# Optimization experiments

Hardware: AMD Instinct MI355X
Metric: run time of the kernel (lower is better)

The kernel has to match this reference:

```python
import jax, jax.numpy as jnp
import numpy as np

B, H, W, D, C = 2, 128, 128, 8, 64
HEADS, DIM_HEAD = 4, 16
F_IN = C * D            # 512
F_OUT = DIM_HEAD * HEADS * D  # 512


def setup_inputs() -> dict:
    key = jax.random.key(0)
    ks = jax.random.split(key, 8)
    s = 0.02
    return {
        "x_in": jax.random.normal(ks[0], (B, H, W, D, C), dtype=jnp.float32),
        "Wq": jax.random.normal(ks[1], (F_IN, F_OUT), dtype=jnp.float32) * s,
        "Wk": jax.random.normal(ks[2], (F_IN, F_OUT), dtype=jnp.float32) * s,
        "Wv": jax.random.normal(ks[3], (F_IN, F_OUT), dtype=jnp.float32) * s,
        "rescale": jnp.ones((HEADS, 1, 1), dtype=jnp.float32),
        "Wp": jax.random.normal(ks[4], (F_OUT, F_IN), dtype=jnp.float32) * s,
        "bp": jnp.zeros((F_IN,), dtype=jnp.float32),
        "pos_w1": jax.random.normal(ks[5], (C, 1, 3, 3, 3), dtype=jnp.float32) * s,
        "pos_w2": jax.random.normal(ks[6], (C, 1, 3, 3, 3), dtype=jnp.float32) * s,
    }


def _dwconv3d(y, kern, groups):
    # y: [b,c,d,h,w], kern: [c,1,3,3,3] depthwise
    return jax.lax.conv_general_dilated(
        y, kern, window_strides=(1, 1, 1), padding="SAME",
        feature_group_count=groups,
        dimension_numbers=("NCDHW", "OIDHW", "NCDHW"))


def reference(x_in, Wq, Wk, Wv, rescale, Wp, bp, pos_w1, pos_w2):
    b, h, w, d, c = x_in.shape
    heads = rescale.shape[0]
    n = h * w
    x = x_in.reshape(b, n, d * c)
    q_inp = x @ Wq
    k_inp = x @ Wk
    v_inp = x @ Wv

    def split(t):  # [b,n,heads*Dh] -> [b,heads,Dh,n]  (Dh = dim_head*num_frm)
        return t.reshape(b, n, heads, -1).transpose(0, 2, 3, 1)

    q, k, v = split(q_inp), split(k_inp), split(v_inp)
    # L2-normalize along spatial axis n (last dim), torch F.normalize eps=1e-12
    q = q / jnp.maximum(jnp.linalg.norm(q, axis=-1, keepdims=True), 1e-12)
    k = k / jnp.maximum(jnp.linalg.norm(k, axis=-1, keepdims=True), 1e-12)
    # channel attention: [b,heads,Dh,Dh]
    attn = jnp.einsum("bhdn,bhen->bhde", k, q) * rescale
    attn = jax.nn.softmax(attn, axis=-1)
    out = jnp.einsum("bhde,bhen->bhdn", attn, v)  # [b,heads,Dh,n]
    out = out.transpose(0, 3, 1, 2).reshape(b, n, -1)  # [b,n,heads*Dh]
    out_c = (out @ Wp + bp).reshape(b, h, w, d, c)

    # positional branch: depthwise conv3d over [b,c,d,h,w]
    vp = v_inp.reshape(b, h, w, d, c).transpose(0, 4, 3, 1, 2)
    p = _dwconv3d(vp, pos_w1, c)
    p = jax.nn.gelu(p, approximate=False)
    p = _dwconv3d(p, pos_w2, c)
    out_p = p.transpose(0, 3, 4, 2, 1)  # -> [b,h,w,d,c]
    return out_c + out_p
```

## Files before the change

### kernel.cpp

```cpp
#include <hip/hip_runtime.h>
#include <math.h>
#include <stdint.h>


using short8  = __attribute__((ext_vector_type(8))) short;
using f32x4   = __attribute__((ext_vector_type(4))) float;

__device__ __forceinline__ float bf2f(unsigned short u) {
  union { unsigned int i; float f; } v; v.i = ((unsigned int)u) << 16; return v.f;
}
__device__ __forceinline__ unsigned short f2bf(float f) {
  union { float f; unsigned int i; } v; v.f = f;
  unsigned int r = v.i + 0x7fffu + ((v.i >> 16) & 1u);
  return (unsigned short)(r >> 16);
}

__device__ __forceinline__ void g2l16(const void* g, void* l) {
  __builtin_amdgcn_global_load_lds(
      (__attribute__((address_space(1))) void*)(unsigned long long)(uintptr_t)g,
      (__attribute__((address_space(3))) void*)(unsigned int)(uintptr_t)l,
      16, 0, 0);
}

__device__ __forceinline__ float fast_gelu(float x) {
  float y = fabsf(x) * 0.70710678118654752f;
  float t = __builtin_amdgcn_rcpf(1.0f + 0.3275911f * y);
  float p = ((((1.061405429f * t - 1.453152027f) * t + 1.421413741f) * t
              - 0.284496736f) * t + 0.254829592f) * t;
  float er = 1.0f - p * __expf(-y * y);
  er = copysignf(er, x);
  return 0.5f * x * (1.0f + er);
}

__global__ __launch_bounds__(256) void convert_x(const float* __restrict__ x,
                                                 unsigned short* __restrict__ xb) {
  int i = (blockIdx.x * 256 + threadIdx.x) * 8;
  float4 a = *(const float4*)&x[i];
  float4 b = *(const float4*)&x[i + 4];
  ushort4 o0, o1;
  o0.x = f2bf(a.x); o0.y = f2bf(a.y); o0.z = f2bf(a.z); o0.w = f2bf(a.w);
  o1.x = f2bf(b.x); o1.y = f2bf(b.y); o1.z = f2bf(b.z); o1.w = f2bf(b.w);
  uint4 o; 
  o.x = *(unsigned*)&o0.x; o.y = *(unsigned*)&o0.z;
  o.z = *(unsigned*)&o1.x; o.w = *(unsigned*)&o1.z;
  *(uint4*)&xb[i] = o;
}

__global__ __launch_bounds__(256) void prep_w(const float* __restrict__ Wq,
                                              const float* __restrict__ Wk,
                                              const float* __restrict__ Wv,
                                              const float* __restrict__ Wp,
                                              unsigned short* __restrict__ Wcat_t,
                                              unsigned short* __restrict__ Wp_t) {
  __shared__ unsigned short Ls[32 * 36];
  int bid = blockIdx.x;
  int mat = bid >> 8, tile = bid & 255;
  int tr = (tile >> 4) * 32, tc = (tile & 15) * 32;
  const float* src = (mat == 0) ? Wq : (mat == 1) ? Wk : (mat == 2) ? Wv : Wp;
  int t = threadIdx.x;
  int r = t >> 3, c4 = (t & 7) * 4;
  float4 v = *(const float4*)&src[(tr + r) * 512 + tc + c4];
  Ls[(c4 + 0) * 36 + r] = f2bf(v.x);
  Ls[(c4 + 1) * 36 + r] = f2bf(v.y);
  Ls[(c4 + 2) * 36 + r] = f2bf(v.z);
  Ls[(c4 + 3) * 36 + r] = f2bf(v.w);
  __syncthreads();
  int rn = t >> 3, ck4 = (t & 7) * 4;
  ushort4 o;
  o.x = Ls[rn * 36 + ck4 + 0]; o.y = Ls[rn * 36 + ck4 + 1];
  o.z = Ls[rn * 36 + ck4 + 2]; o.w = Ls[rn * 36 + ck4 + 3];
  unsigned short* dst = (mat < 3)
      ? &Wcat_t[(long)(mat * 512 + tc + rn) * 512 + tr + ck4]
      : &Wp_t[(long)(tc + rn) * 512 + tr + ck4];
  *(ushort4*)dst = o;
}

__global__ __launch_bounds__(256, 2) void qk_gram(
    const unsigned short* __restrict__ x_bf,
    const unsigned short* __restrict__ Wcat_t,
    float* __restrict__ Gp, float* __restrict__ ss) {
  __shared__ unsigned short sh[38912];
  const int mt2 = blockIdx.x, h = blockIdx.y, b = blockIdx.z;
  const int t = threadIdx.x;
  const int lane = t & 63, w = t >> 6;
  const int wm = w >> 1, wn = w & 1;
  const int quad = lane >> 4, l16 = lane & 15;
  const int sr2 = lane >> 2, sc2 = lane & 3;
  const unsigned short* Bq = Wcat_t + (long)(h * 128) * 512;
  const unsigned short* Bk = Wcat_t + (long)(512 + h * 128) * 512;

  f32x4 g[4][4] = {};

  for (int half = 0; half < 2; half++) {
    const unsigned short* A = x_bf + ((long)b * 16384 + (mt2 * 2 + half) * 128) * 512;
    f32x4 aq[4][4] = {}, ak[4][4] = {};

    auto stage = [&](int k0, int d) {
      unsigned short* Sa = sh + d * 12288;
      unsigned short* Sq = Sa + 4096;
      unsigned short* Sk = Sa + 8192;
#pragma unroll
      for (int q = 0; q < 2; q++) {
        int r = q * 64 + w * 16 + sr2;
        int ca = (sc2 ^ (sr2 & 3)) * 8;
        long off = (long)r * 512 + k0 + ca;
        int ldsb = (q * 64 + w * 16) * 32;
        g2l16(&A[off],  &Sa[ldsb]);
        g2l16(&Bq[off], &Sq[ldsb]);
        g2l16(&Bk[off], &Sk[ldsb]);
      }
    };

    stage(0, 0);
    __syncthreads();
    for (int ks = 0; ks < 16; ks++) {
      int d = ks & 1;
      if (ks < 15) stage((ks + 1) * 32, d ^ 1);
      const unsigned short* Sa = sh + d * 12288;
      const unsigned short* Sq = Sa + 4096;
      const unsigned short* Sk = Sa + 8192;
      short8 af[4], bq4[4], bk4[4];
#pragma unroll
      for (int i = 0; i < 4; i++) {
        int r = wm * 64 + i * 16 + l16;
        int s = quad ^ (r & 3);
        af[i] = *(const short8*)&Sa[r * 32 + s * 8];
      }
#pragma unroll
      for (int j = 0; j < 4; j++) {
        int r = wn * 64 + j * 16 + l16;
        int s = quad ^ (r & 3);
        bq4[j] = *(const short8*)&Sq[r * 32 + s * 8];
        bk4[j] = *(const short8*)&Sk[r * 32 + s * 8];
      }
#pragma unroll
      for (int i = 0; i < 4; i++)
#pragma unroll
        for (int j = 0; j < 4; j++) {
          aq[i][j] = __builtin_amdgcn_mfma_f32_16x16x32_bf16(af[i], bq4[j], aq[i][j], 0, 0, 0);
          ak[i][j] = __builtin_amdgcn_mfma_f32_16x16x32_bf16(af[i], bk4[j], ak[i][j], 0, 0, 0);
        }
      __syncthreads();
    }

    unsigned short* kT = sh;
    unsigned short* qT = sh + 17408;
    float* red = (float*)(sh + 34816);
#pragma unroll
    for (int i = 0; i < 4; i++) {
      int mm = wm * 64 + i * 16 + quad * 4;
#pragma unroll
      for (int j = 0; j < 4; j++) {
        int f = wn * 64 + j * 16 + l16;
        ushort4 oq = { f2bf(aq[i][j][0]), f2bf(aq[i][j][1]), f2bf(aq[i][j][2]), f2bf(aq[i][j][3]) };
        ushort4 ok = { f2bf(ak[i][j][0]), f2bf(ak[i][j][1]), f2bf(ak[i][j][2]), f2bf(ak[i][j][3]) };
        *(ushort4*)&qT[f * 136 + mm] = oq;
        *(ushort4*)&kT[f * 136 + mm] = ok;
      }
    }
    int grp = wm * 4 + quad;
#pragma unroll
    for (int j = 0; j < 4; j++) {
      float pq = 0.f, pk = 0.f;
#pragma unroll
      for (int i = 0; i < 4; i++)
#pragma unroll
        for (int r = 0; r < 4; r++) { pq += aq[i][j][r] * aq[i][j][r]; pk += ak[i][j][r] * ak[i][j][r]; }
      int col = wn * 64 + j * 16 + l16;
      red[grp * 128 + col] = pq;
      red[1024 + grp * 128 + col] = pk;
    }
    __syncthreads();
#pragma unroll
    for (int kk2 = 0; kk2 < 4; kk2++) {
      short8 afk[4], bfq[4];
#pragma unroll
      for (int i = 0; i < 4; i++)
        afk[i] = *(const short8*)&kT[(wm * 64 + i * 16 + l16) * 136 + kk2 * 32 + quad * 8];
#pragma unroll
      for (int j = 0; j < 4; j++)
        bfq[j] = *(const short8*)&qT[(wn * 64 + j * 16 + l16) * 136 + kk2 * 32 + quad * 8];
#pragma unroll
      for (int i = 0; i < 4; i++)
#pragma unroll
        for (int j = 0; j < 4; j++)
          g[i][j] = __builtin_amdgcn_mfma_f32_16x16x32_bf16(afk[i], bfq[j], g[i][j], 0, 0, 0);
    }
    {
      int sel = t >> 7, col = t & 127;
      float s = 0.f;
#pragma unroll
      for (int g2 = 0; g2 < 8; g2++) s += red[sel * 1024 + g2 * 128 + col];
      atomicAdd(&ss[b * 1024 + sel * 512 + h * 128 + col], s);
    }
    __syncthreads();
  }

  float* gp = Gp + (((long)(b * 64 + mt2) * 4 + h) << 14);
#pragma unroll
  for (int i = 0; i < 4; i++) {
    int dd = wm * 64 + i * 16 + quad * 4;
#pragma unroll
    for (int j = 0; j < 4; j++) {
      int e = wn * 64 + j * 16 + l16;
      *(f32x4*)&gp[e * 128 + dd] = g[i][j];
    }
  }
}

__global__ __launch_bounds__(256, 3) void v_gemm(
    const unsigned short* __restrict__ x_bf,
    const unsigned short* __restrict__ Wcat_t,
    unsigned short* __restrict__ v) {
  __shared__ unsigned short As[8192];
  __shared__ unsigned short Bs[8192];
  const int mt = blockIdx.x, nt = blockIdx.y, b = blockIdx.z;
  const int t = threadIdx.x;
  const int lane = t & 63, w = t >> 6;
  const int wm = w >> 1, wn = w & 1;
  const int quad = lane >> 4, l16 = lane & 15;
  const int sr = lane >> 3, sc = lane & 7;
  const unsigned short* A  = x_bf + ((long)b * 16384 + mt * 128) * 512;
  const unsigned short* Bt = Wcat_t + (long)(1024 + nt * 128) * 512;

  f32x4 acc[4][4] = {};
  for (int k0 = 0; k0 < 512; k0 += 64) {
#pragma unroll
    for (int q = 0; q < 4; q++) {
      int r = q * 32 + w * 8 + sr;
      int ca = (sc ^ sr) * 8;
      g2l16(&A[(long)r * 512 + k0 + ca],  &As[(q * 32 + w * 8) * 64]);
      g2l16(&Bt[(long)r * 512 + k0 + ca], &Bs[(q * 32 + w * 8) * 64]);
    }
    __syncthreads();
#pragma unroll
    for (int kk = 0; kk < 2; kk++) {
      short8 af[4], bf[4];
#pragma unroll
      for (int i = 0; i < 4; i++) {
        int r = wm * 64 + i * 16 + l16;
        int s = (kk * 4 + quad) ^ (r & 7);
        af[i] = *(const short8*)&As[r * 64 + s * 8];
      }
#pragma unroll
      for (int j = 0; j < 4; j++) {
        int r = wn * 64 + j * 16 + l16;
        int s = (kk * 4 + quad) ^ (r & 7);
        bf[j] = *(const short8*)&Bs[r * 64 + s * 8];
      }
#pragma unroll
      for (int i = 0; i < 4; i++)
#pragma unroll
        for (int j = 0; j < 4; j++)
          acc[i][j] = __builtin_amdgcn_mfma_f32_16x16x32_bf16(bf[j], af[i], acc[i][j], 0, 0, 0);
    }
    __syncthreads();
  }
  unsigned short* vout = v + ((long)b * 16384 + mt * 128) * 512 + nt * 128;
#pragma unroll
  for (int i = 0; i < 4; i++) {
    long rbase = (long)(wm * 64 + i * 16 + l16) * 512;
#pragma unroll
    for (int j = 0; j < 4; j++) {
      int col = wn * 64 + j * 16 + quad * 4;
      uint2 o;
      o.x = (unsigned)f2bf(acc[i][j][0]) | ((unsigned)f2bf(acc[i][j][1]) << 16);
      o.y = (unsigned)f2bf(acc[i][j][2]) | ((unsigned)f2bf(acc[i][j][3]) << 16);
      *(uint2*)&vout[rbase + col] = o;
    }
  }
}

__global__ __launch_bounds__(256) void reduce_g(const float* __restrict__ Gp,
                                                float* __restrict__ G) {
  int i = blockIdx.x * 256 + threadIdx.x;
  int b = i >> 16, h = (i >> 14) & 3, r = i & 16383;
  const float* p = Gp + (((long)b * 256 + h) << 14) + r;
  float s = 0.f;
#pragma unroll 8
  for (int mtv = 0; mtv < 64; mtv++) s += p[(long)mtv * 65536];
  G[i] = s;
}

__global__ __launch_bounds__(256) void softmax_kernel(const float* __restrict__ Gt,
                                                      const float* __restrict__ ss,
                                                      const float* __restrict__ rescale,
                                                      unsigned short* __restrict__ Abd) {
  __shared__ float L[128 * 129];
  __shared__ float rsq[128];
  __shared__ float rsk[128];
  int h = blockIdx.x, b = blockIdx.y;
  int t = threadIdx.x;
  const float* g = Gt + (long)(b * 4 + h) * 16384;
  if (t < 128) rsq[t] = rsqrtf(fmaxf(ss[b * 1024 + h * 128 + t], 1e-24f));
  else { int d = t - 128; rsk[d] = rsqrtf(fmaxf(ss[b * 1024 + 512 + h * 128 + d], 1e-24f)); }
  __syncthreads();
  float rs = rescale[h];
  for (int i = t; i < 16384; i += 256) {
    int e = i >> 7, d = i & 127;
    L[d * 129 + e] = g[i] * rsk[d] * rsq[e] * rs;
  }
  __syncthreads();
  if (t < 128) {
    float* row = &L[t * 129];
    float mx = -1e30f;
    for (int e = 0; e < 128; e++) mx = fmaxf(mx, row[e]);
    float sum = 0.0f;
    for (int e = 0; e < 128; e++) { float ex = __expf(row[e] - mx); row[e] = ex; sum += ex; }
    float inv = 1.0f / sum;
    long abase = (long)b * 262144;
    for (int e = 0; e < 128; e++)
      Abd[abase + (long)(h * 128 + e) * 512 + h * 128 + t] = f2bf(row[e] * inv);
  }
}

__global__ __launch_bounds__(256, 3) void gemm_lds(
    const unsigned short* __restrict__ A, const unsigned short* __restrict__ Bt,
    unsigned short* __restrict__ C, const float* __restrict__ bias,
    int lda, int ldb, int ldc, int K, long sA, long sB, long sC) {
  __shared__ unsigned short As[128 * 64];
  __shared__ unsigned short Bs[128 * 64];
  const int t = threadIdx.x;
  const int m0 = blockIdx.x * 128, n0 = blockIdx.y * 128;
  A  += (long)blockIdx.z * sA + (long)m0 * lda;
  Bt += (long)blockIdx.z * sB + (long)n0 * ldb;
  C  += (long)blockIdx.z * sC;
  const int lane = t & 63, w = t >> 6;
  const int wm = w >> 1, wn = w & 1;
  const int quad = lane >> 4, l16 = lane & 15;
  const int sr = lane >> 3, sc = lane & 7;

  f32x4 acc[4][4] = {};

  for (int k0 = 0; k0 < K; k0 += 64) {
#pragma unroll
    for (int q = 0; q < 4; q++) {
      int r = q * 32 + w * 8 + sr;
      int ca = (sc ^ sr) * 8;
      g2l16(&A[(long)r * lda + k0 + ca], &As[(q * 32 + w * 8) * 64]);
      g2l16(&Bt[(long)r * ldb + k0 + ca], &Bs[(q * 32 + w * 8) * 64]);
    }
    __syncthreads();
#pragma unroll
    for (int kk = 0; kk < 2; kk++) {
      short8 af[4], bfq[4];
#pragma unroll
      for (int i = 0; i < 4; i++) {
        int r = wm * 64 + i * 16 + l16;
        int s = (kk * 4 + quad) ^ (r & 7);
        af[i] = *(const short8*)&As[r * 64 + s * 8];
      }
#pragma unroll
      for (int j = 0; j < 4; j++) {
        int r = wn * 64 + j * 16 + l16;
        int s = (kk * 4 + quad) ^ (r & 7);
        bfq[j] = *(const short8*)&Bs[r * 64 + s * 8];
      }
#pragma unroll
      for (int i = 0; i < 4; i++)
#pragma unroll
        for (int j = 0; j < 4; j++)
          acc[i][j] = __builtin_amdgcn_mfma_f32_16x16x32_bf16(bfq[j], af[i], acc[i][j], 0, 0, 0);
    }
    __syncthreads();
  }

#pragma unroll
  for (int i = 0; i < 4; i++) {
    long rbase = (long)(m0 + wm * 64 + i * 16 + l16) * ldc;
#pragma unroll
    for (int j = 0; j < 4; j++) {
      int col = n0 + wn * 64 + j * 16 + quad * 4;
      float b0 = 0.f, b1 = 0.f, b2 = 0.f, b3 = 0.f;
      if (bias) { float4 bv = *(const float4*)&bias[col]; b0 = bv.x; b1 = bv.y; b2 = bv.z; b3 = bv.w; }
      uint2 o;
      o.x = (unsigned)f2bf(acc[i][j][0] + b0) | ((unsigned)f2bf(acc[i][j][1] + b1) << 16);
      o.y = (unsigned)f2bf(acc[i][j][2] + b2) | ((unsigned)f2bf(acc[i][j][3] + b3) << 16);
      *(uint2*)&C[rbase + col] = o;
    }
  }
}

template <bool GELU>
__global__ __launch_bounds__(256) void dwconv_kernel(
    const unsigned short* __restrict__ in,
    const float* __restrict__ wgt,
    const unsigned short* __restrict__ addc,
    unsigned short* __restrict__ outb,
    float* __restrict__ outf) {
  __shared__ unsigned short tile[60 * 512];
  __shared__ float wl[27 * 64];
  int wt = blockIdx.x, ht = blockIdx.y, b = blockIdx.z;
  int t = threadIdx.x;
  for (int i = t; i < 1728; i += 256) {
    int c = i / 27, tap = i % 27;
    wl[tap * 64 + c] = wgt[i];
  }
  int h0 = ht * 4, w0 = wt * 8;
  int lg = t & 63;
#pragma unroll 5
  for (int rr = 0; rr < 15; rr++) {
    int row = rr * 4 + (t >> 6);
    int hh = row / 10, ww = row % 10;
    int gh = h0 + hh - 1, gw = w0 + ww - 1;
    uint4 vv = {0u, 0u, 0u, 0u};
    if ((unsigned)gh < 128u && (unsigned)gw < 128u)
      vv = *(const uint4*)&in[((long)(b * 16384 + gh * 128 + gw)) * 512 + lg * 8];
    *(uint4*)&tile[row * 512 + lg * 8] = vv;
  }
  __syncthreads();

  int f0 = lg * 8;
  int d = f0 >> 6, c0 = f0 & 63;
  int pg = t >> 6;
  int pwb = (pg & 1) * 4;
#pragma unroll
  for (int P = 0; P < 2; P++) {
    int ph = P * 2 + (pg >> 1);
    float acc[4][8] = {};
    for (int kd = 0; kd < 3; kd++) {
      int dz = d + kd - 1;
      if ((unsigned)dz >= 8u) continue;
      int fz = dz * 64 + c0;
#pragma unroll
      for (int kh = 0; kh < 3; kh++) {
        float tf[6][8];
#pragma unroll
        for (int cc = 0; cc < 6; cc++) {
          uint4 pv = *(const uint4*)&tile[((ph + kh) * 10 + pwb + cc) * 512 + fz];
          const unsigned short* u = (const unsigned short*)&pv;
#pragma unroll
          for (int j = 0; j < 8; j++) tf[cc][j] = bf2f(u[j]);
        }
#pragma unroll
        for (int kw = 0; kw < 3; kw++) {
          int tap = kd * 9 + kh * 3 + kw;
          float wv[8];
          *(float4*)&wv[0] = *(const float4*)&wl[tap * 64 + c0];
          *(float4*)&wv[4] = *(const float4*)&wl[tap * 64 + c0 + 4];
#pragma unroll
          for (int s = 0; s < 4; s++)
#pragma unroll
            for (int j = 0; j < 8; j++) acc[s][j] += tf[s + kw][j] * wv[j];
        }
      }
    }
#pragma unroll
    for (int s = 0; s < 4; s++) {
      int pw = pwb + s;
      long row = (long)(b * 16384 + (h0 + ph) * 128 + (w0 + pw));
      if (GELU) {
        unsigned short o[8];
#pragma unroll
        for (int j = 0; j < 8; j++) o[j] = f2bf(fast_gelu(acc[s][j]));
        *(uint4*)&outb[row * 512 + f0] = *(uint4*)&o[0];
      } else {
        uint4 av = *(const uint4*)&addc[row * 512 + f0];
        const unsigned short* au = (const unsigned short*)&av;
        float o[8];
#pragma unroll
        for (int j = 0; j < 8; j++) o[j] = acc[s][j] + bf2f(au[j]);
        *(float4*)&outf[row * 512 + f0]     = *(float4*)&o[0];
        *(float4*)&outf[row * 512 + f0 + 4] = *(float4*)&o[4];
      }
    }
  }
}

extern "C" void kernel_launch(void* const* d_in, const int* in_sizes, int n_in,
                              void* d_out, int out_size, void* d_ws, size_t ws_size,
                              hipStream_t stream) {
  const float* x   = (const float*)d_in[0];
  const float* Wq  = (const float*)d_in[1];
  const float* Wk  = (const float*)d_in[2];
  const float* Wv  = (const float*)d_in[3];
  const float* rsc = (const float*)d_in[4];
  const float* Wp  = (const float*)d_in[5];
  const float* bp  = (const float*)d_in[6];
  const float* pw1 = (const float*)d_in[7];
  const float* pw2 = (const float*)d_in[8];
  float* out = (float*)d_out;

  char* ws = (char*)d_ws;
  unsigned short* x_bf   = (unsigned short*)(ws + 0);
  unsigned short* v      = (unsigned short*)(ws + 33554432);
  unsigned short* out_c  = (unsigned short*)(ws + 67108864);
  float*          Gp     = (float*)(ws + 100663296);
  unsigned short* Wcat_t = (unsigned short*)(ws + 167772160);
  unsigned short* Wp_t   = (unsigned short*)(ws + 169345024);
  float*          ss     = (float*)(ws + 169869312);
  float*          G      = (float*)(ws + 169877504);
  unsigned short* Abd    = (unsigned short*)(ws + 170401792);
  unsigned short* Mt     = (unsigned short*)(ws + 171450368);
  unsigned short* p1     = x_bf;

  hipMemsetAsync(ss, 0, 8192, stream);
  hipMemsetAsync(Abd, 0, 1048576, stream);

  convert_x<<<8192, 256, 0, stream>>>(x, x_bf);
  prep_w<<<1024, 256, 0, stream>>>(Wq, Wk, Wv, Wp, Wcat_t, Wp_t);

  qk_gram<<<dim3(64, 4, 2), 256, 0, stream>>>(x_bf, Wcat_t, Gp, ss);
  v_gemm<<<dim3(128, 4, 2), 256, 0, stream>>>(x_bf, Wcat_t, v);

  reduce_g<<<512, 256, 0, stream>>>(Gp, G);
  softmax_kernel<<<dim3(4, 2, 1), 256, 0, stream>>>(G, ss, rsc, Abd);

  gemm_lds<<<dim3(4, 4, 2), 256, 0, stream>>>(
      Wp_t, Abd, Mt, nullptr, 512, 512, 512, 512, 0L, 262144L, 262144L);

  gemm_lds<<<dim3(128, 4, 2), 256, 0, stream>>>(
      v, Mt, out_c, bp, 512, 512, 512, 512,
      (long)16384 * 512, 262144L, (long)16384 * 512);

  dwconv_kernel<true><<<dim3(16, 32, 2), 256, 0, stream>>>(
      v, pw1, nullptr, p1, nullptr);
  dwconv_kernel<false><<<dim3(16, 32, 2), 256, 0, stream>>>(
      p1, pw2, out_c, nullptr, out);
}
```

Measured before the change: 349.0 us.

## Drop LDS halo tile in depthwise conv, read neighbors directly from global

The depthwise 3D conv no longer stages a 6x10 halo tile of 512 features into shared memory. Each thread now reads its six neighboring columns straight from global memory per (kh,kd) and accumulates 4 outputs along w. The grid becomes one row per block with 16 columns, and launch bounds request 4 blocks per CU. This removes the ~60KB LDS footprint and its barrier to raise occupancy, in exchange for more redundant global/L2 reads across the h and d neighbors.

```diff
diff --git a/kernel.cpp b/kernel.cpp
--- a/kernel.cpp
+++ b/kernel.cpp
@@ -382,87 +382,84 @@
 }
 
 template <bool GELU>
-__global__ __launch_bounds__(256) void dwconv_kernel(
+__global__ __launch_bounds__(256, 4) void dwconv_kernel(
     const unsigned short* __restrict__ in,
     const float* __restrict__ wgt,
     const unsigned short* __restrict__ addc,
     unsigned short* __restrict__ outb,
     float* __restrict__ outf) {
-  __shared__ unsigned short tile[60 * 512];
   __shared__ float wl[27 * 64];
-  int wt = blockIdx.x, ht = blockIdx.y, b = blockIdx.z;
   int t = threadIdx.x;
   for (int i = t; i < 1728; i += 256) {
     int c = i / 27, tap = i % 27;
     wl[tap * 64 + c] = wgt[i];
   }
-  int h0 = ht * 4, w0 = wt * 8;
-  int lg = t & 63;
-#pragma unroll 5
-  for (int rr = 0; rr < 15; rr++) {
-    int row = rr * 4 + (t >> 6);
-    int hh = row / 10, ww = row % 10;
-    int gh = h0 + hh - 1, gw = w0 + ww - 1;
-    uint4 vv = {0u, 0u, 0u, 0u};
-    if ((unsigned)gh < 128u && (unsigned)gw < 128u)
-      vv = *(const uint4*)&in[((long)(b * 16384 + gh * 128 + gw)) * 512 + lg * 8];
-    *(uint4*)&tile[row * 512 + lg * 8] = vv;
-  }
   __syncthreads();
-
-  int f0 = lg * 8;
-  int d = f0 >> 6, c0 = f0 & 63;
-  int pg = t >> 6;
-  int pwb = (pg & 1) * 4;
-#pragma unroll
-  for (int P = 0; P < 2; P++) {
-    int ph = P * 2 + (pg >> 1);
-    float acc[4][8] = {};
+  int h = blockIdx.y, b = blockIdx.z;
+  int fg = t & 63, q = t >> 6;
+  int w0 = blockIdx.x * 16 + q * 4;
+  int f0 = fg * 8;
+  int d = f0 >> 6, cch = f0 & 63;
+
+  float acc[4][8] = {};
+#pragma unroll
+  for (int kh = 0; kh < 3; kh++) {
+    int gh = h + kh - 1;
+    if ((unsigned)gh >= 128u) continue;
+    long rbase = (long)(b * 16384 + gh * 128);
+#pragma unroll
     for (int kd = 0; kd < 3; kd++) {
       int dz = d + kd - 1;
       if ((unsigned)dz >= 8u) continue;
-      int fz = dz * 64 + c0;
-#pragma unroll
-      for (int kh = 0; kh < 3; kh++) {
-        float tf[6][8];
-#pragma unroll
-        for (int cc = 0; cc < 6; cc++) {
-          uint4 pv = *(const uint4*)&tile[((ph + kh) * 10 + pwb + cc) * 512 + fz];
-          const unsigned short* u = (const unsigned short*)&pv;
-#pragma unroll
-          for (int j = 0; j < 8; j++) tf[cc][j] = bf2f(u[j]);
+      int fz = dz * 64 + cch;
+      float wv[3][8];
+#pragma unroll
+      for (int kw = 0; kw < 3; kw++) {
+        int tap = kd * 9 + kh * 3 + kw;
+        *(float4*)&wv[kw][0] = *(const float4*)&wl[tap * 64 + cch];
+        *(float4*)&wv[kw][4] = *(const float4*)&wl[tap * 64 + cch + 4];
+      }
+      uint4 rr[6];
+#pragma unroll
+      for (int cc = 0; cc < 6; cc++) {
+        int gw = w0 + cc - 1;
+        uint4 vv = {0u, 0u, 0u, 0u};
+        if ((unsigned)gw < 128u)
+          vv = *(const uint4*)&in[(rbase + gw) * 512 + fz];
+        rr[cc] = vv;
+      }
+#pragma unroll
+      for (int cc = 0; cc < 6; cc++) {
+        const unsigned short* u = (const unsigned short*)&rr[cc];
+        float tf[8];
+#pragma unroll
+        for (int j = 0; j < 8; j++) tf[j] = bf2f(u[j]);
+#pragma unroll
+        for (int kw = 0; kw < 3; kw++) {
+          int s = cc - kw;
+          if (s < 0 || s > 3) continue;
+#pragma unroll
+          for (int j = 0; j < 8; j++) acc[s][j] += tf[j] * wv[kw][j];
         }
-#pragma unroll
-        for (int kw = 0; kw < 3; kw++) {
-          int tap = kd * 9 + kh * 3 + kw;
-          float wv[8];
-          *(float4*)&wv[0] = *(const float4*)&wl[tap * 64 + c0];
-          *(float4*)&wv[4] = *(const float4*)&wl[tap * 64 + c0 + 4];
-#pragma unroll
-          for (int s = 0; s < 4; s++)
-#pragma unroll
-            for (int j = 0; j < 8; j++) acc[s][j] += tf[s + kw][j] * wv[j];
-        }
-      }
-    }
-#pragma unroll
-    for (int s = 0; s < 4; s++) {
-      int pw = pwb + s;
-      long row = (long)(b * 16384 + (h0 + ph) * 128 + (w0 + pw));
-      if (GELU) {
-        unsigned short o[8];
-#pragma unroll
-        for (int j = 0; j < 8; j++) o[j] = f2bf(fast_gelu(acc[s][j]));
-        *(uint4*)&outb[row * 512 + f0] = *(uint4*)&o[0];
-      } else {
-        uint4 av = *(const uint4*)&addc[row * 512 + f0];
-        const unsigned short* au = (const unsigned short*)&av;
-        float o[8];
-#pragma unroll
-        for (int j = 0; j < 8; j++) o[j] = acc[s][j] + bf2f(au[j]);
-        *(float4*)&outf[row * 512 + f0]     = *(float4*)&o[0];
-        *(float4*)&outf[row * 512 + f0 + 4] = *(float4*)&o[4];
-      }
+      }
+    }
+  }
+#pragma unroll
+  for (int s = 0; s < 4; s++) {
+    long row = (long)(b * 16384 + h * 128 + (w0 + s));
+    if (GELU) {
+      unsigned short o[8];
+#pragma unroll
+      for (int j = 0; j < 8; j++) o[j] = f2bf(fast_gelu(acc[s][j]));
+      *(uint4*)&outb[row * 512 + f0] = *(uint4*)&o[0];
+    } else {
+      uint4 av = *(const uint4*)&addc[row * 512 + f0];
+      const unsigned short* au = (const unsigned short*)&av;
+      float o[8];
+#pragma unroll
+      for (int j = 0; j < 8; j++) o[j] = acc[s][j] + bf2f(au[j]);
+      *(float4*)&outf[row * 512 + f0]     = *(float4*)&o[0];
+      *(float4*)&outf[row * 512 + f0 + 4] = *(float4*)&o[4];
     }
   }
 }
@@ -513,8 +510,8 @@
       v, Mt, out_c, bp, 512, 512, 512, 512,
       (long)16384 * 512, 262144L, (long)16384 * 512);
 
-  dwconv_kernel<true><<<dim3(16, 32, 2), 256, 0, stream>>>(
+  dwconv_kernel<true><<<dim3(8, 128, 2), 256, 0, stream>>>(
       v, pw1, nullptr, p1, nullptr);
-  dwconv_kernel<false><<<dim3(16, 32, 2), 256, 0, stream>>>(
+  dwconv_kernel<false><<<dim3(8, 128, 2), 256, 0, stream>>>(
       p1, pw2, out_c, nullptr, out);
 }
```

Result: no change. 351.6 us (+0.7%).
